# Performance work log

Hardware: AMD Instinct MI355X
Metric: run time of the kernel (lower is better)

## Reference

```python
import jax, jax.numpy as jnp
import numpy as np

QMAX = 127.0  # int8 symmetric

def fake_quant(v):
    # symmetric per-tensor int8 quant -> dequant
    s = jnp.maximum(jnp.max(jnp.abs(v)), 1e-8) / QMAX
    return jnp.round(jnp.clip(v / s, -QMAX, QMAX)) * s

def setup_inputs() -> dict:
    key = jax.random.key(0)
    k1, k2, k3 = jax.random.split(key, 3)
    B, C, H, W = 64, 3, 224, 224
    D, P = 768, 8
    x = jax.random.normal(k1, (B, C, H, W), dtype=jnp.float32)
    w = jax.random.normal(k2, (D, C, P, P), dtype=jnp.float32) * 0.02
    b = jax.random.normal(k3, (D,), dtype=jnp.float32) * 0.02
    return {"x": x, "w": w, "b": b}

def reference(x, w, b):
    B, C, H, W = x.shape
    D, _, P, _ = w.shape
    gh, gw = H // P, W // P
    # quantized conv (HMQConv2d): fake-quant activations and weights, then patchify GEMM
    xq = fake_quant(x)
    wq = fake_quant(w)
    # extract non-overlapping PxP patches: [B, C, gh, P, gw, P]
    xp = xq.reshape(B, C, gh, P, gw, P)
    # conv stride=kernel=P  ==  patch matmul: out [B, gh, gw, D]
    out = jnp.einsum('bchpwq,dchq->bhwd', xp.transpose(0, 1, 2, 3, 4, 5), wq,
                     optimize=True) if False else jnp.einsum('bcxpyq,dcpq->bxyd', xp, wq)
    out = out + b
    # flatten(2).transpose(1,2): [B, N, D]
    out = out.reshape(B, gh * gw, D)
    # norm is Identity (norm_layer=None)
    return out
```

## Files before the change

### kernel.cpp

```cpp
#include <hip/hip_runtime.h>
#include <stdint.h>


typedef short bf16x8 __attribute__((ext_vector_type(8)));
using f32x4 = __attribute__((ext_vector_type(4))) float;

static __device__ __forceinline__ uint16_t f2bfbits(float f) {
  uint32_t u = __float_as_uint(f);
  u += 0x7FFFu + ((u >> 16) & 1u);
  return (uint16_t)(u >> 16);
}
static __device__ __forceinline__ uint32_t q2(float a, float b, float inv_s) {
  float qa = rintf(fminf(fmaxf(a * inv_s, -127.0f), 127.0f));
  float qb = rintf(fminf(fmaxf(b * inv_s, -127.0f), 127.0f));
  return (uint32_t)f2bfbits(qa) | ((uint32_t)f2bfbits(qb) << 16);
}
static __device__ __forceinline__ uint4 quant8(float4 a0, float4 a1, float inv_s) {
  uint4 q;
  q.x = q2(a0.x, a0.y, inv_s);
  q.y = q2(a0.z, a0.w, inv_s);
  q.z = q2(a1.x, a1.y, inv_s);
  q.w = q2(a1.z, a1.w, inv_s);
  return q;
}

#define NBX 1024
#define NBW 64
__global__ void absmax_k(const float4* __restrict__ x, int nx4,
                         const float4* __restrict__ w, int nw4,
                         float* __restrict__ partials) {
  __shared__ float red[4];
  float m = 0.0f;
  if (blockIdx.x < NBX) {
    for (int i = blockIdx.x * 256 + threadIdx.x; i < nx4; i += NBX * 256) {
      float4 u = x[i];
      m = fmaxf(m, fabsf(u.x)); m = fmaxf(m, fabsf(u.y));
      m = fmaxf(m, fabsf(u.z)); m = fmaxf(m, fabsf(u.w));
    }
  } else {
    for (int i = (blockIdx.x - NBX) * 256 + threadIdx.x; i < nw4; i += NBW * 256) {
      float4 u = w[i];
      m = fmaxf(m, fabsf(u.x)); m = fmaxf(m, fabsf(u.y));
      m = fmaxf(m, fabsf(u.z)); m = fmaxf(m, fabsf(u.w));
    }
  }
#pragma unroll
  for (int off = 32; off > 0; off >>= 1) m = fmaxf(m, __shfl_down(m, off, 64));
  if ((threadIdx.x & 63) == 0) red[threadIdx.x >> 6] = m;
  __syncthreads();
  if (threadIdx.x == 0) {
    m = fmaxf(fmaxf(red[0], red[1]), fmaxf(red[2], red[3]));
    partials[blockIdx.x] = m;
  }
}

#define NQXB 1792
#define NQWB 72
__global__ __launch_bounds__(256) void quant_xw_k(
    const float* __restrict__ x, const float4* __restrict__ w4,
    uint4* __restrict__ Aq, uint4* __restrict__ Wq,
    const float* __restrict__ partials, float* __restrict__ slots) {
  __shared__ float redx[4];
  __shared__ float redw_s;
  __shared__ uint4 stg[28 * 25];
  const int tid = threadIdx.x;

  float mx = 0.0f;
  for (int i = tid; i < NBX; i += 256) mx = fmaxf(mx, partials[i]);
#pragma unroll
  for (int off = 32; off > 0; off >>= 1) mx = fmaxf(mx, __shfl_down(mx, off, 64));
  if ((tid & 63) == 0) redx[tid >> 6] = mx;
  if (tid < 64) {
    float mw = partials[NBX + tid];
#pragma unroll
    for (int off = 32; off > 0; off >>= 1) mw = fmaxf(mw, __shfl_down(mw, off, 64));
    if (tid == 0) redw_s = mw;
  }
  __syncthreads();
  float sx = fmaxf(fmaxf(redx[0], redx[1]), fmaxf(redx[2], redx[3]));
  sx = fmaxf(sx, 1e-8f) * (1.0f / 127.0f);
  float sw = fmaxf(redw_s, 1e-8f) * (1.0f / 127.0f);
  if (blockIdx.x == 0 && tid == 0) { slots[0] = sx; slots[1] = sw; }

  if (blockIdx.x < NQXB) {
    const float inv = 1.0f / sx;
    const int b  = blockIdx.x / 28;
    const int gx = blockIdx.x - b * 28;
    for (int t = tid; t < 672; t += 256) {
      const int r  = t / 28;
      const int gy = t - r * 28;
      const int c = r >> 3, p = r & 7;
      const float4* src =
          (const float4*)(x + (size_t)((b * 3 + c) * 224 + gx * 8 + p) * 224);
      float4 a0 = src[gy * 2], a1 = src[gy * 2 + 1];
      stg[gy * 25 + r] = quant8(a0, a1, inv);
    }
    __syncthreads();
    uint4* dst = Aq + (size_t)(b * 784 + gx * 28) * 24;
    for (int t = tid; t < 672; t += 256) {
      const int gy = t / 24;
      dst[t] = stg[gy * 25 + (t - gy * 24)];
    }
  } else {
    const float inv = 1.0f / sw;
    const int g = (blockIdx.x - NQXB) * 256 + tid;
    float4 a0 = w4[g * 2], a1 = w4[g * 2 + 1];
    Wq[g] = quant8(a0, a1, inv);
  }
}

__global__ __launch_bounds__(256) void gemm_k(
    const uint4* __restrict__ Aq, const uint4* __restrict__ Wq,
    const float* __restrict__ bias, const float* __restrict__ slots,
    float* __restrict__ out) {
  __shared__ float tr[4 * 1280];
  const int tid  = threadIdx.x;
  const int lane = tid & 63;
  const int wid  = tid >> 6;
  const int wm   = wid >> 1;
  const int wn   = wid & 1;
  const int lm   = lane & 15;
  const int lq   = lane >> 4;
  const int m0   = blockIdx.x * 128;
  const int n0   = blockIdx.y * 128;

  int abase[4], bbase[4];
#pragma unroll
  for (int tm = 0; tm < 4; ++tm)
    abase[tm] = (m0 + wm * 64 + tm * 16 + lm) * 24 + lq;
#pragma unroll
  for (int tn = 0; tn < 4; ++tn)
    bbase[tn] = (n0 + wn * 64 + tn * 16 + lm) * 24 + lq;

  f32x4 acc[4][4] = {};

#pragma unroll
  for (int ks = 0; ks < 6; ++ks) {
    bf16x8 af[4], bf[4];
#pragma unroll
    for (int tm = 0; tm < 4; ++tm)
      af[tm] = __builtin_bit_cast(bf16x8, Aq[abase[tm] + ks * 4]);
#pragma unroll
    for (int tn = 0; tn < 4; ++tn)
      bf[tn] = __builtin_bit_cast(bf16x8, Wq[bbase[tn] + ks * 4]);
#pragma unroll
    for (int tm = 0; tm < 4; ++tm)
#pragma unroll
      for (int tn = 0; tn < 4; ++tn)
        acc[tm][tn] = __builtin_amdgcn_mfma_f32_16x16x32_bf16(
            af[tm], bf[tn], acc[tm][tn], 0, 0, 0);
  }

  const float scale = slots[0] * slots[1];
  float* T = &tr[wid * 1280];
  const int c4 = lane & 15;
  const int gc = n0 + wn * 64 + c4 * 4;
  const float4 bv = *(const float4*)&bias[gc];

#pragma unroll
  for (int tm = 0; tm < 4; ++tm) {
#pragma unroll
    for (int tn = 0; tn < 4; ++tn)
      *(f32x4*)&T[(tn * 16 + lm) * 20 + lq * 4] = acc[tm][tn];
    asm volatile("s_waitcnt lgkmcnt(0)" ::: "memory");
#pragma unroll
    for (int i = 0; i < 4; ++i) {
      const int s = (lane >> 4) + i * 4;
      float4 v;
      v.x = T[(c4 * 4 + 0) * 20 + s];
      v.y = T[(c4 * 4 + 1) * 20 + s];
      v.z = T[(c4 * 4 + 2) * 20 + s];
      v.w = T[(c4 * 4 + 3) * 20 + s];
      float4 o;
      o.x = fmaf(v.x, scale, bv.x);
      o.y = fmaf(v.y, scale, bv.y);
      o.z = fmaf(v.z, scale, bv.z);
      o.w = fmaf(v.w, scale, bv.w);
      const int gm = m0 + wm * 64 + tm * 16 + s;
      *(float4*)&out[(size_t)gm * 768 + gc] = o;
    }
    asm volatile("s_waitcnt lgkmcnt(0)" ::: "memory");
  }
}


extern "C" void kernel_launch(void* const* d_in, const int* in_sizes, int n_in,
                              void* d_out, int out_size, void* d_ws, size_t ws_size,
                              hipStream_t stream) {
  const float* xf = (const float*)d_in[0];
  const float4* x4 = (const float4*)d_in[0];
  const float4* w4 = (const float4*)d_in[1];
  const float* bias = (const float*)d_in[2];
  float* out = (float*)d_out;

  char* ws = (char*)d_ws;
  float* slots    = (float*)ws;
  float* partials = (float*)(ws + 256);
  uint4* Wq       = (uint4*)(ws + 8192);
  uint4* Aq       = (uint4*)(ws + 8192 + 294912);

  const int nx4 = 9633792 / 4;
  const int nw4 = 147456 / 4;

  absmax_k<<<NBX + NBW, 256, 0, stream>>>(x4, nx4, w4, nw4, partials);
  quant_xw_k<<<NQXB + NQWB, 256, 0, stream>>>(xf, w4, Aq, Wq, partials, slots);
  gemm_k<<<dim3(392, 6), 256, 0, stream>>>(Aq, Wq, bias, slots, out);
}
```

Baseline: 232.7 us.

## Switch quantized GEMM from bf16 to int8 MFMA with int8 staging

```diff
diff --git a/kernel.cpp b/kernel.cpp
--- a/kernel.cpp
+++ b/kernel.cpp
@@ -2,26 +2,18 @@
 #include <stdint.h>
 
 
-typedef short bf16x8 __attribute__((ext_vector_type(8)));
 using f32x4 = __attribute__((ext_vector_type(4))) float;
-
-static __device__ __forceinline__ uint16_t f2bfbits(float f) {
-  uint32_t u = __float_as_uint(f);
-  u += 0x7FFFu + ((u >> 16) & 1u);
-  return (uint16_t)(u >> 16);
-}
-static __device__ __forceinline__ uint32_t q2(float a, float b, float inv_s) {
-  float qa = rintf(fminf(fmaxf(a * inv_s, -127.0f), 127.0f));
-  float qb = rintf(fminf(fmaxf(b * inv_s, -127.0f), 127.0f));
-  return (uint32_t)f2bfbits(qa) | ((uint32_t)f2bfbits(qb) << 16);
-}
-static __device__ __forceinline__ uint4 quant8(float4 a0, float4 a1, float inv_s) {
-  uint4 q;
-  q.x = q2(a0.x, a0.y, inv_s);
-  q.y = q2(a0.z, a0.w, inv_s);
-  q.z = q2(a1.x, a1.y, inv_s);
-  q.w = q2(a1.z, a1.w, inv_s);
-  return q;
+using i32x4 = __attribute__((ext_vector_type(4))) int;
+
+static __device__ __forceinline__ uint32_t q4i8(float4 v, float inv_s) {
+  uint32_t r;
+  int q0 = (int)rintf(fminf(fmaxf(v.x * inv_s, -127.0f), 127.0f));
+  int q1 = (int)rintf(fminf(fmaxf(v.y * inv_s, -127.0f), 127.0f));
+  int q2 = (int)rintf(fminf(fmaxf(v.z * inv_s, -127.0f), 127.0f));
+  int q3 = (int)rintf(fminf(fmaxf(v.w * inv_s, -127.0f), 127.0f));
+  r = (uint32_t)(q0 & 0xff) | ((uint32_t)(q1 & 0xff) << 8) |
+      ((uint32_t)(q2 & 0xff) << 16) | ((uint32_t)(q3 & 0xff) << 24);
+  return r;
 }
 
 #define NBX 1024
@@ -55,14 +47,14 @@
 }
 
 #define NQXB 1792
-#define NQWB 72
+#define NQWB 36
 __global__ __launch_bounds__(256) void quant_xw_k(
     const float* __restrict__ x, const float4* __restrict__ w4,
     uint4* __restrict__ Aq, uint4* __restrict__ Wq,
     const float* __restrict__ partials, float* __restrict__ slots) {
   __shared__ float redx[4];
   __shared__ float redw_s;
-  __shared__ uint4 stg[28 * 25];
+  __shared__ uint2 stg8[28][26];
   const int tid = threadIdx.x;
 
   float mx = 0.0f;
@@ -93,19 +85,29 @@
       const float4* src =
           (const float4*)(x + (size_t)((b * 3 + c) * 224 + gx * 8 + p) * 224);
       float4 a0 = src[gy * 2], a1 = src[gy * 2 + 1];
-      stg[gy * 25 + r] = quant8(a0, a1, inv);
+      uint2 q;
+      q.x = q4i8(a0, inv);
+      q.y = q4i8(a1, inv);
+      stg8[gy][r] = q;
     }
     __syncthreads();
-    uint4* dst = Aq + (size_t)(b * 784 + gx * 28) * 24;
-    for (int t = tid; t < 672; t += 256) {
-      const int gy = t / 24;
-      dst[t] = stg[gy * 25 + (t - gy * 24)];
+    uint4* dst = Aq + (size_t)(b * 784 + gx * 28) * 12;
+    for (int t = tid; t < 336; t += 256) {
+      const int gy = t / 12;
+      const int j  = t - gy * 12;
+      uint2 lo = stg8[gy][2 * j], hi = stg8[gy][2 * j + 1];
+      uint4 v; v.x = lo.x; v.y = lo.y; v.z = hi.x; v.w = hi.y;
+      dst[t] = v;
     }
   } else {
     const float inv = 1.0f / sw;
     const int g = (blockIdx.x - NQXB) * 256 + tid;
-    float4 a0 = w4[g * 2], a1 = w4[g * 2 + 1];
-    Wq[g] = quant8(a0, a1, inv);
+    float4 a0 = w4[g * 4], a1 = w4[g * 4 + 1];
+    float4 a2 = w4[g * 4 + 2], a3 = w4[g * 4 + 3];
+    uint4 q;
+    q.x = q4i8(a0, inv); q.y = q4i8(a1, inv);
+    q.z = q4i8(a2, inv); q.w = q4i8(a3, inv);
+    Wq[g] = q;
   }
 }
 
@@ -127,27 +129,27 @@
   int abase[4], bbase[4];
 #pragma unroll
   for (int tm = 0; tm < 4; ++tm)
-    abase[tm] = (m0 + wm * 64 + tm * 16 + lm) * 24 + lq;
+    abase[tm] = (m0 + wm * 64 + tm * 16 + lm) * 12 + lq;
 #pragma unroll
   for (int tn = 0; tn < 4; ++tn)
-    bbase[tn] = (n0 + wn * 64 + tn * 16 + lm) * 24 + lq;
-
-  f32x4 acc[4][4] = {};
-
-#pragma unroll
-  for (int ks = 0; ks < 6; ++ks) {
-    bf16x8 af[4], bf[4];
+    bbase[tn] = (n0 + wn * 64 + tn * 16 + lm) * 12 + lq;
+
+  i32x4 acc[4][4] = {};
+
+#pragma unroll
+  for (int ks = 0; ks < 3; ++ks) {
+    i32x4 af[4], bf[4];
 #pragma unroll
     for (int tm = 0; tm < 4; ++tm)
-      af[tm] = __builtin_bit_cast(bf16x8, Aq[abase[tm] + ks * 4]);
+      af[tm] = __builtin_bit_cast(i32x4, Aq[abase[tm] + ks * 4]);
 #pragma unroll
     for (int tn = 0; tn < 4; ++tn)
-      bf[tn] = __builtin_bit_cast(bf16x8, Wq[bbase[tn] + ks * 4]);
+      bf[tn] = __builtin_bit_cast(i32x4, Wq[bbase[tn] + ks * 4]);
 #pragma unroll
     for (int tm = 0; tm < 4; ++tm)
 #pragma unroll
       for (int tn = 0; tn < 4; ++tn)
-        acc[tm][tn] = __builtin_amdgcn_mfma_f32_16x16x32_bf16(
+        acc[tm][tn] = __builtin_amdgcn_mfma_i32_16x16x64_i8(
             af[tm], bf[tn], acc[tm][tn], 0, 0, 0);
   }
 
@@ -160,8 +162,12 @@
 #pragma unroll
   for (int tm = 0; tm < 4; ++tm) {
 #pragma unroll
-    for (int tn = 0; tn < 4; ++tn)
-      *(f32x4*)&T[(tn * 16 + lm) * 20 + lq * 4] = acc[tm][tn];
+    for (int tn = 0; tn < 4; ++tn) {
+      f32x4 f;
+#pragma unroll
+      for (int j = 0; j < 4; ++j) f[j] = (float)acc[tm][tn][j];
+      *(f32x4*)&T[(tn * 16 + lm) * 20 + lq * 4] = f;
+    }
     asm volatile("s_waitcnt lgkmcnt(0)" ::: "memory");
 #pragma unroll
     for (int i = 0; i < 4; ++i) {
@@ -197,7 +203,7 @@
   float* slots    = (float*)ws;
   float* partials = (float*)(ws + 256);
   uint4* Wq       = (uint4*)(ws + 8192);
-  uint4* Aq       = (uint4*)(ws + 8192 + 294912);
+  uint4* Aq       = (uint4*)(ws + 8192 + 147456);
 
   const int nx4 = 9633792 / 4;
   const int nw4 = 147456 / 4;
```

Result: faster. 200.3 us (-13.9%).
